# Optimization experiments

Measured on AMD Instinct MI355X. Metric: run time of the kernel, lower is better.

Reference implementation:

```python
import jax, jax.numpy as jnp
import numpy as np

B, L, D, H = 8, 1024, 768, 12
UNITS, NHEADS, HDIM = 768, 12, 64
R = 0.5  # ours_force_reduction_ratio
NEG = jnp.finfo(jnp.float32).min


def setup_inputs() -> dict:
    key = jax.random.key(0)
    ks = jax.random.split(key, 12)
    hidden_states = jax.random.normal(ks[0], (B, L, D), jnp.float32)
    # HF-style extended attention mask [B,1,1,L]: 0 for valid, big negative for padding
    lengths = jax.random.randint(ks[1], (B,), L // 2, L + 1)
    pos = jnp.arange(L)
    attention_mask = jnp.where(pos[None, :] < lengths[:, None], 0.0, -1e9).astype(jnp.float32).reshape(B, 1, 1, L)
    self_attention_scores = jax.random.uniform(ks[2], (B, H, L, L), dtype=jnp.float32)
    key_layer = jax.random.normal(ks[3], (B, H, L, HDIM), jnp.float32)  # unused by forward
    tome_size = jnp.ones((B, L, 1), jnp.float32)  # unused by forward (recomputed)
    s = 0.02
    Wq = jax.random.normal(ks[4], (D, UNITS), jnp.float32) * s
    Wk = jax.random.normal(ks[5], (D, UNITS), jnp.float32) * s
    Wv = jax.random.normal(ks[6], (D, UNITS), jnp.float32) * s
    Wo = jax.random.normal(ks[7], (UNITS, D), jnp.float32) * s
    bq = jnp.zeros((UNITS,), jnp.float32)
    bk = jnp.zeros((UNITS,), jnp.float32)
    bv = jnp.zeros((UNITS,), jnp.float32)
    bo = jnp.zeros((D,), jnp.float32)
    return dict(hidden_states=hidden_states, attention_mask=attention_mask,
                self_attention_scores=self_attention_scores, key_layer=key_layer,
                tome_size=tome_size, Wq=Wq, bq=bq, Wk=Wk, bk=bk, Wv=Wv, bv=bv, Wo=Wo, bo=bo)


def _mha(q, kv, key_padding_mask, Wq, bq, Wk, bk, Wv, bv, Wo, bo):
    # standard multi-head cross attention; q: [B,Lq,D], kv: [B,L,D]
    Bq, Lq, _ = q.shape
    Q = (q @ Wq + bq).reshape(Bq, Lq, NHEADS, HDIM)
    Kp = (kv @ Wk + bk).reshape(Bq, -1, NHEADS, HDIM)
    Vp = (kv @ Wv + bv).reshape(Bq, -1, NHEADS, HDIM)
    scores = jnp.einsum('bqhd,bkhd->bhqk', Q, Kp) / jnp.sqrt(jnp.float32(HDIM))
    if key_padding_mask is not None:
        scores = jnp.where(key_padding_mask[:, None, None, :], NEG, scores)
    att = jax.nn.softmax(scores, axis=-1)
    out = jnp.einsum('bhqk,bkhd->bqhd', att, Vp).reshape(Bq, Lq, UNITS)
    return out @ Wo + bo


def reference(hidden_states, attention_mask, self_attention_scores, key_layer, tome_size,
              Wq, bq, Wk, bk, Wv, bv, Wo, bo):
    # per-sample variable K = floor(valid_len * R) - num_new_token, clamped to >= 1
    valid = (attention_mask > -10.0).astype(hidden_states.dtype)  # [B,1,1,L]
    K_list = (valid.reshape(B, L).sum(-1) * R).astype(jnp.int32)
    K_list = jnp.maximum(K_list - 1, 1)  # num_new_token == 1
    # masked_attention_scores: outer product of the 0/1 mask applied per head
    m = valid.reshape(B, L)
    scores = self_attention_scores * (m[:, :, None] * m[:, None, :])[:, None, :, :]
    imp = scores.mean(axis=1).mean(axis=1)  # mean over heads then queries -> [B,L]
    imp = imp.at[:, 0].set(jnp.inf)  # always preserve CLS
    # rank of each token in descending importance (double argsort)
    order = jnp.argsort(-imp, axis=-1)
    rank = jnp.argsort(order, axis=-1)
    keep = rank < K_list[:, None]  # [B,L]; topk_attention_mask == ~keep
    preserved_attention_mask = jnp.where(keep[:, None, None, :], attention_mask, NEG)
    # sentence pooling via softmax over the extended mask
    att = jax.nn.softmax(attention_mask, axis=-1).reshape(B, 1, L)
    sentences = jnp.einsum('bql,bld->bqd', att, hidden_states)  # [B,1,D]
    key_padding_mask = attention_mask.reshape(B, L) < -10.0
    new_token = _mha(sentences, hidden_states, key_padding_mask, Wq, bq, Wk, bk, Wv, bv, Wo, bo)
    final_token = jnp.concatenate([hidden_states, new_token], axis=1)  # [B,L+1,D]
    new_attention_mask = jnp.zeros((B, 1, 1, 1), hidden_states.dtype)
    final_attention_mask = jnp.concatenate([preserved_attention_mask, new_attention_mask], axis=-1)
    tome = jnp.ones((B, L + 1, 1), hidden_states.dtype)
    return final_token, final_attention_mask, tome
```

## Files before the change

kernel.cpp:

```cpp
#include <hip/hip_runtime.h>
#include <math.h>

#define Bb 8
#define Ll 1024
#define Dd 768
#define Hh 12
#define ROWS7 32
#define QS 8
#define SS 8
#define WSC 16
#define DC 24

#define NIMP (Bb*Hh*QS)
#define NSENT (Bb*SS)
#define NCOPY4 (Bb*Ll*Dd/4)
#define NTOME4 (Bb*(Ll+1)/4)
#define NCPYBLK ((NCOPY4 + NTOME4 + 255)/256)
#define GRID_A (NIMP + NSENT + NCPYBLK + 1)

__device__ __constant__ float NEGF_ = -3.0e38f;

#define OFF_COUNTS   0
#define OFF_QPART    256
#define OFF_QV       (OFF_QPART + DC*Bb*Dd*4)
#define OFF_U        (OFF_QV + Bb*Dd*4)
#define OFF_SBUF     (OFF_U + Bb*Hh*Dd*4)
#define OFF_SENTP    (OFF_SBUF + (size_t)Bb*Hh*Ll*4)
#define OFF_PART     (OFF_SENTP + Bb*SS*Dd*8)
#define OFF_WPART    (OFF_PART + (size_t)Bb*Hh*QS*Ll*4)
#define OFF_OPART    (OFF_WPART + (size_t)Bb*WSC*Hh*Dd*4)
#define OFF_NPART    (OFF_OPART + DC*Bb*Dd*4)

__device__ __forceinline__ int block_count256(const float* __restrict__ amask_b, int t) {
    int c = 0;
    #pragma unroll
    for (int i = 0; i < 4; ++i)
        c += (amask_b[t + 256*i] > -10.0f) ? 1 : 0;
    #pragma unroll
    for (int off = 32; off; off >>= 1) c += __shfl_xor(c, off, 64);
    __shared__ int cred[4];
    if ((t & 63) == 0) cred[t >> 6] = c;
    __syncthreads();
    return cred[0] + cred[1] + cred[2] + cred[3];
}

__global__ void kA_mega(const float4* __restrict__ scores4, const float* __restrict__ amask,
                        const float4* __restrict__ hid4,
                        float4* __restrict__ part4, double* __restrict__ sentp,
                        int* __restrict__ counts, float4* __restrict__ out4) {
    int blk = blockIdx.x;
    int t = threadIdx.x;
    if (blk < NIMP) {
        int b = blk / (Hh*QS);
        int rem = blk % (Hh*QS);
        int h = rem / QS, c = rem % QS;
        int count = block_count256(amask + b*Ll, t);
        int rpc = (count + QS - 1) / QS;
        int q0 = c*rpc, q1 = min(q0 + rpc, count);
        if (4*t >= count) return;
        const float4* base = scores4 + ((size_t)(b*Hh + h)*Ll)*(Ll/4) + t;
        float ax=0.f, ay=0.f, az=0.f, aw=0.f;
        float bx=0.f, by=0.f, bz=0.f, bw=0.f;
        int q = q0;
        #pragma unroll 4
        for (; q + 1 < q1; q += 2) {
            float4 v0 = base[(size_t)q*(Ll/4)];
            float4 v1 = base[(size_t)(q+1)*(Ll/4)];
            ax += v0.x; ay += v0.y; az += v0.z; aw += v0.w;
            bx += v1.x; by += v1.y; bz += v1.z; bw += v1.w;
        }
        if (q < q1) {
            float4 v = base[(size_t)q*(Ll/4)];
            ax += v.x; ay += v.y; az += v.z; aw += v.w;
        }
        float4 o; o.x = ax+bx; o.y = ay+by; o.z = az+bz; o.w = aw+bw;
        part4[(size_t)(b*(Hh*QS) + rem)*(Ll/4) + t] = o;
    } else if (blk < NIMP + NSENT) {
        int blk2 = blk - NIMP;
        int b = blk2 / SS, c = blk2 % SS;
        int count = block_count256(amask + b*Ll, t);
        int rpc = (count + SS - 1) / SS;
        int l0 = c*rpc, l1 = min(l0 + rpc, count);
        if (t < 192) {
            double a0=0, a1=0, a2=0, a3=0;
            const float4* base = hid4 + (size_t)b*Ll*(Dd/4) + t;
            #pragma unroll 4
            for (int l = l0; l < l1; ++l) {
                float4 v = base[(size_t)l*(Dd/4)];
                a0 += (double)v.x; a1 += (double)v.y; a2 += (double)v.z; a3 += (double)v.w;
            }
            double* o = sentp + (size_t)(b*SS + c)*Dd + 4*t;
            o[0]=a0; o[1]=a1; o[2]=a2; o[3]=a3;
        }
    } else if (blk < NIMP + NSENT + NCPYBLK) {
        int idx = (blk - NIMP - NSENT)*256 + t;
        if (idx < NCOPY4) {
            int b = idx / (Ll*Dd/4), r = idx % (Ll*Dd/4);
            out4[(size_t)b*((Ll+1)*Dd/4) + r] = hid4[idx];
        } else if (idx < NCOPY4 + NTOME4) {
            float4 one; one.x=one.y=one.z=one.w = 1.0f;
            out4[(size_t)(Bb*(Ll+1)*Dd + Bb*(Ll+1))/4 + (idx - NCOPY4)] = one;
        }
    } else {
        int w = t >> 6, lane = t & 63;
        for (int b = w; b < Bb; b += 4) {
            int c = 0;
            #pragma unroll
            for (int i = 0; i < 16; ++i)
                c += (amask[b*Ll + lane + 64*i] > -10.0f) ? 1 : 0;
            #pragma unroll
            for (int off = 32; off; off >>= 1) c += __shfl_xor(c, off, 64);
            if (lane == 0) counts[b] = c;
        }
    }
}

__global__ void kB_rank(const float* __restrict__ part, const int* __restrict__ counts,
                        const float* __restrict__ amask, float* __restrict__ out_mask) {
    __shared__ double simp[Ll];
    int blk = blockIdx.x;
    int b = blk >> 4, seg = blk & 15;
    int t = threadIdx.x;
    int count = counts[b];
    #pragma unroll
    for (int i = 0; i < 4; ++i) {
        int k = t + 256*i;
        double v;
        if (k == 0) v = 1.0e300;
        else if (k < count) {
            double s = 0.0;
            #pragma unroll 4
            for (int j = 0; j < Hh*QS; ++j)
                s += (double)part[(size_t)(b*(Hh*QS) + j)*Ll + k];
            v = s * (1.0/12288.0);
        } else v = 0.0;
        simp[k] = v;
    }
    __syncthreads();
    int K = max((count >> 1) - 1, 1);
    int ti = seg*64 + (t >> 2);
    int prt = t & 3;
    double mv = simp[ti];
    int cnt = 0;
    int l0 = prt*256;
    #pragma unroll 4
    for (int j = 0; j < 256; ++j) {
        int l = l0 + j;
        double v = simp[l];
        cnt += (v > mv || (v == mv && l < ti)) ? 1 : 0;
    }
    cnt += __shfl_xor(cnt, 1, 64);
    cnt += __shfl_xor(cnt, 2, 64);
    if (prt == 0)
        out_mask[b*(Ll+1) + ti] = (cnt < K) ? amask[b*Ll + ti] : NEGF_;
    if (seg == 0 && t == 0) out_mask[b*(Ll+1) + Ll] = 0.0f;
}

__global__ void kC_qpart(const double* __restrict__ sentp, const int* __restrict__ counts,
                         const float* __restrict__ Wq, float* __restrict__ qpart) {
    __shared__ float s_lds[Bb][32];
    int blk = blockIdx.x, t = threadIdx.x;
    int d0 = blk*32;
    {
        int b = t >> 5, dd = t & 31;
        double s = 0.0;
        #pragma unroll
        for (int c = 0; c < SS; ++c)
            s += sentp[(size_t)(b*SS + c)*Dd + d0 + dd];
        s_lds[b][dd] = (float)(s / (double)counts[b]);
    }
    __syncthreads();
    float acc[Bb][3];
    #pragma unroll
    for (int b = 0; b < Bb; ++b) { acc[b][0]=0.f; acc[b][1]=0.f; acc[b][2]=0.f; }
    #pragma unroll 4
    for (int dd = 0; dd < 32; ++dd) {
        const float* wr = Wq + (size_t)(d0 + dd)*Dd;
        float w0 = wr[t], w1 = wr[t+256], w2 = wr[t+512];
        #pragma unroll
        for (int b = 0; b < Bb; ++b) {
            float sv = s_lds[b][dd];
            acc[b][0] += sv*w0; acc[b][1] += sv*w1; acc[b][2] += sv*w2;
        }
    }
    #pragma unroll
    for (int b = 0; b < Bb; ++b) {
        float* o = qpart + (size_t)(blk*Bb + b)*Dd;
        o[t] = acc[b][0]; o[t+256] = acc[b][1]; o[t+512] = acc[b][2];
    }
}

__global__ void kD_u(const float* __restrict__ qpart, const float* __restrict__ bq,
                     const float* __restrict__ Wk,
                     float* __restrict__ Qv, float* __restrict__ u) {
    __shared__ float q_lds[64];
    int blk = blockIdx.x; int b = blk / Hh, h = blk % Hh;
    int t = threadIdx.x;
    if (t < 64) {
        int j = h*64 + t;
        float s = 0.f;
        #pragma unroll
        for (int c = 0; c < DC; ++c) s += qpart[(size_t)(c*Bb + b)*Dd + j];
        s += bq[j];
        q_lds[t] = s;
        Qv[b*Dd + j] = s;
    }
    __syncthreads();
    #pragma unroll
    for (int i = 0; i < 3; ++i) {
        int d = t + 256*i;
        const float* wr = Wk + (size_t)d*Dd + h*64;
        float acc = 0.f;
        #pragma unroll
        for (int j = 0; j < 64; ++j) acc += wr[j]*q_lds[j];
        u[(size_t)(b*Hh + h)*Dd + d] = acc;
    }
}

__global__ void kE_scores(const float4* __restrict__ hid4, const float4* __restrict__ u4,
                          const float* __restrict__ Qv, const float* __restrict__ bk,
                          const int* __restrict__ counts, float* __restrict__ sbuf) {
    __shared__ float4 u_lds[Hh*192];
    __shared__ float qbk[Hh];
    int blk = blockIdx.x;
    int b = blk / (Ll/ROWS7);
    int kc = blk % (Ll/ROWS7);
    int t = threadIdx.x;
    for (int i = t; i < Hh*192; i += 256) u_lds[i] = u4[(size_t)b*Hh*192 + i];
    if (t < Hh) {
        float a = 0.f;
        for (int j = 0; j < 64; ++j) a += Qv[b*Dd + t*64 + j] * bk[t*64 + j];
        qbk[t] = a;
    }
    __syncthreads();
    int count = counts[b];
    int wave = t >> 6, lane = t & 63;
    #pragma unroll
    for (int r = 0; r < ROWS7/4; ++r) {
        int k = kc*ROWS7 + wave + 4*r;
        const float4* hr4 = hid4 + (size_t)(b*Ll + k)*(Dd/4) + lane;
        float a[Hh];
        #pragma unroll
        for (int h = 0; h < Hh; ++h) a[h] = 0.f;
        #pragma unroll
        for (int i = 0; i < 3; ++i) {
            float4 v = hr4[i*64];
            #pragma unroll
            for (int h = 0; h < Hh; ++h) {
                float4 uv = u_lds[h*192 + i*64 + lane];
                a[h] += v.x*uv.x + v.y*uv.y + v.z*uv.z + v.w*uv.w;
            }
        }
        #pragma unroll
        for (int h = 0; h < Hh; ++h) {
            #pragma unroll
            for (int off = 32; off; off >>= 1) a[h] += __shfl_xor(a[h], off, 64);
        }
        #pragma unroll
        for (int h = 0; h < Hh; ++h) {
            if (lane == h) {
                sbuf[(size_t)(b*Hh + h)*Ll + k] =
                    (k < count) ? (a[h] + qbk[h]) * 0.125f : -1.0e30f;
            }
        }
    }
}

__global__ void kF_softmax(float* __restrict__ sbuf) {
    __shared__ float redmax[4];
    __shared__ float redsum[4];
    int blk = blockIdx.x, t = threadIdx.x;
    float* s = sbuf + (size_t)blk * Ll;
    int wave = t >> 6, lane = t & 63;
    float v0 = s[t], v1 = s[t+256], v2 = s[t+512], v3 = s[t+768];
    float mx = fmaxf(fmaxf(v0, v1), fmaxf(v2, v3));
    #pragma unroll
    for (int off = 32; off; off >>= 1) mx = fmaxf(mx, __shfl_xor(mx, off, 64));
    if (lane == 0) redmax[wave] = mx;
    __syncthreads();
    mx = fmaxf(fmaxf(redmax[0], redmax[1]), fmaxf(redmax[2], redmax[3]));
    float e0 = expf(v0-mx), e1 = expf(v1-mx), e2 = expf(v2-mx), e3 = expf(v3-mx);
    float sum = e0+e1+e2+e3;
    #pragma unroll
    for (int off = 32; off; off >>= 1) sum += __shfl_xor(sum, off, 64);
    if (lane == 0) redsum[wave] = sum;
    __syncthreads();
    sum = redsum[0]+redsum[1]+redsum[2]+redsum[3];
    s[t]     = e0/sum;
    s[t+256] = e1/sum;
    s[t+512] = e2/sum;
    s[t+768] = e3/sum;
}

__global__ void kG_wpart(const float4* __restrict__ hid4, const float* __restrict__ att,
                         const int* __restrict__ counts, float4* __restrict__ wpart4) {
    __shared__ float att_s[Hh][64];
    int blk = blockIdx.x;
    int b = blk / WSC, c = blk % WSC;
    int count = counts[b];
    int rpc = (count + WSC - 1) / WSC;
    int l0 = c*rpc, l1 = min(l0 + rpc, count);
    int nl = l1 - l0;
    int t = threadIdx.x;
    for (int idx = t; idx < Hh*64; idx += 192) {
        int h = idx >> 6, ll = idx & 63;
        att_s[h][ll] = (ll < nl) ? att[(size_t)(b*Hh + h)*Ll + l0 + ll] : 0.f;
    }
    __syncthreads();
    float4 acc[Hh];
    #pragma unroll
    for (int h = 0; h < Hh; ++h) { acc[h].x=0.f; acc[h].y=0.f; acc[h].z=0.f; acc[h].w=0.f; }
    const float4* base = hid4 + (size_t)b*Ll*(Dd/4) + t;
    #pragma unroll 2
    for (int l = 0; l < nl; ++l) {
        float4 v = base[(size_t)(l0 + l)*(Dd/4)];
        #pragma unroll
        for (int h = 0; h < Hh; ++h) {
            float ah = att_s[h][l];
            acc[h].x += ah*v.x; acc[h].y += ah*v.y; acc[h].z += ah*v.z; acc[h].w += ah*v.w;
        }
    }
    #pragma unroll
    for (int h = 0; h < Hh; ++h)
        wpart4[((size_t)(b*WSC + c)*Hh + h)*(Dd/4) + t] = acc[h];
}

__global__ void kH_opart(const float* __restrict__ wpart, const float* __restrict__ Wv,
                         float* __restrict__ opart) {
    __shared__ float w_lds[Bb][Hh][32];
    int blk = blockIdx.x, t = threadIdx.x;
    int d0 = blk*32;
    for (int idx = t; idx < Bb*Hh*32; idx += 256) {
        int b = idx / (Hh*32);
        int rem = idx % (Hh*32);
        int h = rem >> 5, dd = rem & 31;
        float s = 0.f;
        #pragma unroll
        for (int c = 0; c < WSC; ++c)
            s += wpart[((size_t)(b*WSC + c)*Hh + h)*Dd + d0 + dd];
        w_lds[b][h][dd] = s;
    }
    __syncthreads();
    int j0 = t, j1 = t+256, j2 = t+512;
    int h0 = j0 >> 6, h1 = j1 >> 6, h2 = j2 >> 6;
    float acc[Bb][3];
    #pragma unroll
    for (int b = 0; b < Bb; ++b) { acc[b][0]=0.f; acc[b][1]=0.f; acc[b][2]=0.f; }
    #pragma unroll 4
    for (int dd = 0; dd < 32; ++dd) {
        const float* wr = Wv + (size_t)(d0 + dd)*Dd;
        float w0 = wr[j0], w1 = wr[j1], w2 = wr[j2];
        #pragma unroll
        for (int b = 0; b < Bb; ++b) {
            acc[b][0] += w_lds[b][h0][dd]*w0;
            acc[b][1] += w_lds[b][h1][dd]*w1;
            acc[b][2] += w_lds[b][h2][dd]*w2;
        }
    }
    #pragma unroll
    for (int b = 0; b < Bb; ++b) {
        float* o = opart + (size_t)(blk*Bb + b)*Dd;
        o[j0] = acc[b][0]; o[j1] = acc[b][1]; o[j2] = acc[b][2];
    }
}

__global__ void kI_npart(const float* __restrict__ opart, const float* __restrict__ bv,
                         const float* __restrict__ Wo, float* __restrict__ npart) {
    __shared__ float o_lds[Bb][32];
    int blk = blockIdx.x, t = threadIdx.x;
    int jr0 = blk*32;
    {
        int b = t >> 5, jj = t & 31;
        int j = jr0 + jj;
        float s = 0.f;
        #pragma unroll
        for (int c = 0; c < DC; ++c) s += opart[(size_t)(c*Bb + b)*Dd + j];
        o_lds[b][jj] = s + bv[j];
    }
    __syncthreads();
    float acc[Bb][3];
    #pragma unroll
    for (int b = 0; b < Bb; ++b) { acc[b][0]=0.f; acc[b][1]=0.f; acc[b][2]=0.f; }
    #pragma unroll 4
    for (int jj = 0; jj < 32; ++jj) {
        const float* wr = Wo + (size_t)(jr0 + jj)*Dd;
        float w0 = wr[t], w1 = wr[t+256], w2 = wr[t+512];
        #pragma unroll
        for (int b = 0; b < Bb; ++b) {
            float ov = o_lds[b][jj];
            acc[b][0] += ov*w0; acc[b][1] += ov*w1; acc[b][2] += ov*w2;
        }
    }
    #pragma unroll
    for (int b = 0; b < Bb; ++b) {
        float* o = npart + (size_t)(blk*Bb + b)*Dd;
        o[t] = acc[b][0]; o[t+256] = acc[b][1]; o[t+512] = acc[b][2];
    }
}

__global__ void kJ_final(const float* __restrict__ npart, const float* __restrict__ bo,
                         float* __restrict__ out) {
    int b = blockIdx.x, t = threadIdx.x;
    size_t base = ((size_t)b*(Ll+1) + Ll)*Dd;
    #pragma unroll
    for (int i = 0; i < 3; ++i) {
        int d = t + 256*i;
        float s = 0.f;
        #pragma unroll
        for (int c = 0; c < DC; ++c) s += npart[(size_t)(c*Bb + b)*Dd + d];
        out[base + d] = s + bo[d];
    }
}

extern "C" void kernel_launch(void* const* d_in, const int* in_sizes, int n_in,
                              void* d_out, int out_size, void* d_ws, size_t ws_size,
                              hipStream_t stream) {
    const float* hidden = (const float*)d_in[0];
    const float* amask  = (const float*)d_in[1];
    const float* scores = (const float*)d_in[2];
    const float* Wq = (const float*)d_in[5];
    const float* bq = (const float*)d_in[6];
    const float* Wk = (const float*)d_in[7];
    const float* bk = (const float*)d_in[8];
    const float* Wv = (const float*)d_in[9];
    const float* bv = (const float*)d_in[10];
    const float* Wo = (const float*)d_in[11];
    const float* bo = (const float*)d_in[12];
    float* out = (float*)d_out;

    char* ws = (char*)d_ws;
    int*    counts = (int*)   (ws + OFF_COUNTS);
    float*  qpart  = (float*) (ws + OFF_QPART);
    float*  Qv     = (float*) (ws + OFF_QV);
    float*  u      = (float*) (ws + OFF_U);
    float*  sbuf   = (float*) (ws + OFF_SBUF);
    double* sentp  = (double*)(ws + OFF_SENTP);
    float*  part   = (float*) (ws + OFF_PART);
    float*  wpart  = (float*) (ws + OFF_WPART);
    float*  opart  = (float*) (ws + OFF_OPART);
    float*  npart  = (float*) (ws + OFF_NPART);

    float* out_mask = out + (size_t)Bb*(Ll+1)*Dd;

    kA_mega   <<<GRID_A, 256, 0, stream>>>((const float4*)scores, amask,
                                           (const float4*)hidden,
                                           (float4*)part, sentp, counts, (float4*)out);
    kB_rank   <<<Bb*16, 256, 0, stream>>>(part, counts, amask, out_mask);
    kC_qpart  <<<DC, 256, 0, stream>>>(sentp, counts, Wq, qpart);
    kD_u      <<<Bb*Hh, 256, 0, stream>>>(qpart, bq, Wk, Qv, u);
    kE_scores <<<Bb*(Ll/ROWS7), 256, 0, stream>>>((const float4*)hidden, (const float4*)u,
                                                  Qv, bk, counts, sbuf);
    kF_softmax<<<Bb*Hh, 256, 0, stream>>>(sbuf);
    kG_wpart  <<<Bb*WSC, 192, 0, stream>>>((const float4*)hidden, sbuf, counts,
                                           (float4*)wpart);
    kH_opart  <<<DC, 256, 0, stream>>>(wpart, Wv, opart);
    kI_npart  <<<DC, 256, 0, stream>>>(opart, bv, Wo, npart);
    kJ_final  <<<Bb, 256, 0, stream>>>(npart, bo, out);
}
```

Baseline: 190.0 us.

## Fuse query projection into u kernel and softmax into weighted-sum kernel

Merges the Wq projection (kC) with the Wk fold (kD) so each (batch, head) block computes its own 64-wide query slice from the pooled sentence. This removes the qpart workspace round-trip and one launch. It also folds the softmax kernel into kG: each block recomputes the per-head max and sum over the score rows and normalizes on the fly, which removes another launch and the rewrite of sbuf. The cost is redundant softmax statistics across the 16 chunk blocks per batch, and a serial 24-step staged loop over Wq in each of 96 blocks.

After: 204.4 us. +7.5%, slower.

```diff
diff --git a/kernel.cpp b/kernel.cpp
--- a/kernel.cpp
+++ b/kernel.cpp
@@ -21,8 +21,7 @@
 __device__ __constant__ float NEGF_ = -3.0e38f;
 
 #define OFF_COUNTS   0
-#define OFF_QPART    256
-#define OFF_QV       (OFF_QPART + DC*Bb*Dd*4)
+#define OFF_QV       256
 #define OFF_U        (OFF_QV + Bb*Dd*4)
 #define OFF_SBUF     (OFF_U + Bb*Hh*Dd*4)
 #define OFF_SENTP    (OFF_SBUF + (size_t)Bb*Hh*Ll*4)
@@ -156,54 +155,48 @@
     if (seg == 0 && t == 0) out_mask[b*(Ll+1) + Ll] = 0.0f;
 }
 
-__global__ void kC_qpart(const double* __restrict__ sentp, const int* __restrict__ counts,
-                         const float* __restrict__ Wq, float* __restrict__ qpart) {
-    __shared__ float s_lds[Bb][32];
-    int blk = blockIdx.x, t = threadIdx.x;
-    int d0 = blk*32;
-    {
-        int b = t >> 5, dd = t & 31;
-        double s = 0.0;
-        #pragma unroll
-        for (int c = 0; c < SS; ++c)
-            s += sentp[(size_t)(b*SS + c)*Dd + d0 + dd];
-        s_lds[b][dd] = (float)(s / (double)counts[b]);
-    }
-    __syncthreads();
-    float acc[Bb][3];
-    #pragma unroll
-    for (int b = 0; b < Bb; ++b) { acc[b][0]=0.f; acc[b][1]=0.f; acc[b][2]=0.f; }
-    #pragma unroll 4
-    for (int dd = 0; dd < 32; ++dd) {
-        const float* wr = Wq + (size_t)(d0 + dd)*Dd;
-        float w0 = wr[t], w1 = wr[t+256], w2 = wr[t+512];
-        #pragma unroll
-        for (int b = 0; b < Bb; ++b) {
-            float sv = s_lds[b][dd];
-            acc[b][0] += sv*w0; acc[b][1] += sv*w1; acc[b][2] += sv*w2;
-        }
-    }
-    #pragma unroll
-    for (int b = 0; b < Bb; ++b) {
-        float* o = qpart + (size_t)(blk*Bb + b)*Dd;
-        o[t] = acc[b][0]; o[t+256] = acc[b][1]; o[t+512] = acc[b][2];
-    }
-}
-
-__global__ void kD_u(const float* __restrict__ qpart, const float* __restrict__ bq,
-                     const float* __restrict__ Wk,
-                     float* __restrict__ Qv, float* __restrict__ u) {
+__global__ void kCD_qu(const double* __restrict__ sentp, const int* __restrict__ counts,
+                       const float* __restrict__ Wq, const float* __restrict__ bq,
+                       const float* __restrict__ Wk,
+                       float* __restrict__ Qv, float* __restrict__ u) {
+    __shared__ float s_lds[Dd];
+    __shared__ float4 wstage[512];
+    __shared__ float qpart_lds[4][64];
     __shared__ float q_lds[64];
     int blk = blockIdx.x; int b = blk / Hh, h = blk % Hh;
     int t = threadIdx.x;
+    double cntd = (double)counts[b];
+    for (int i = t; i < Dd; i += 256) {
+        double s = 0.0;
+        #pragma unroll
+        for (int c = 0; c < SS; ++c) s += sentp[(size_t)(b*SS + c)*Dd + i];
+        s_lds[i] = (float)(s / cntd);
+    }
+    __syncthreads();
+    int lane = t & 63, w = t >> 6;
+    const float4* wq4 = (const float4*)Wq;
+    float qacc = 0.f;
+    for (int it = 0; it < 24; ++it) {
+        int d0 = it*32;
+        #pragma unroll
+        for (int f = t; f < 512; f += 256) {
+            int r = f >> 4, c4 = f & 15;
+            wstage[f] = wq4[(size_t)(d0 + r)*192 + h*16 + c4];
+        }
+        __syncthreads();
+        const float* wsf = (const float*)wstage;
+        #pragma unroll
+        for (int r = w*8; r < w*8 + 8; ++r)
+            qacc += s_lds[d0 + r] * wsf[r*64 + lane];
+        __syncthreads();
+    }
+    qpart_lds[w][lane] = qacc;
+    __syncthreads();
     if (t < 64) {
-        int j = h*64 + t;
-        float s = 0.f;
-        #pragma unroll
-        for (int c = 0; c < DC; ++c) s += qpart[(size_t)(c*Bb + b)*Dd + j];
-        s += bq[j];
-        q_lds[t] = s;
-        Qv[b*Dd + j] = s;
+        float q = qpart_lds[0][t] + qpart_lds[1][t] + qpart_lds[2][t]
+                + qpart_lds[3][t] + bq[h*64 + t];
+        q_lds[t] = q;
+        Qv[b*Dd + h*64 + t] = q;
     }
     __syncthreads();
     #pragma unroll
@@ -266,45 +259,40 @@
     }
 }
 
-__global__ void kF_softmax(float* __restrict__ sbuf) {
-    __shared__ float redmax[4];
-    __shared__ float redsum[4];
-    int blk = blockIdx.x, t = threadIdx.x;
-    float* s = sbuf + (size_t)blk * Ll;
-    int wave = t >> 6, lane = t & 63;
-    float v0 = s[t], v1 = s[t+256], v2 = s[t+512], v3 = s[t+768];
-    float mx = fmaxf(fmaxf(v0, v1), fmaxf(v2, v3));
-    #pragma unroll
-    for (int off = 32; off; off >>= 1) mx = fmaxf(mx, __shfl_xor(mx, off, 64));
-    if (lane == 0) redmax[wave] = mx;
-    __syncthreads();
-    mx = fmaxf(fmaxf(redmax[0], redmax[1]), fmaxf(redmax[2], redmax[3]));
-    float e0 = expf(v0-mx), e1 = expf(v1-mx), e2 = expf(v2-mx), e3 = expf(v3-mx);
-    float sum = e0+e1+e2+e3;
-    #pragma unroll
-    for (int off = 32; off; off >>= 1) sum += __shfl_xor(sum, off, 64);
-    if (lane == 0) redsum[wave] = sum;
-    __syncthreads();
-    sum = redsum[0]+redsum[1]+redsum[2]+redsum[3];
-    s[t]     = e0/sum;
-    s[t+256] = e1/sum;
-    s[t+512] = e2/sum;
-    s[t+768] = e3/sum;
-}
-
-__global__ void kG_wpart(const float4* __restrict__ hid4, const float* __restrict__ att,
-                         const int* __restrict__ counts, float4* __restrict__ wpart4) {
+__global__ void kFG_wpart(const float4* __restrict__ hid4, const float* __restrict__ sbuf,
+                          const int* __restrict__ counts, float4* __restrict__ wpart4) {
+    __shared__ float m_s[Hh], is_s[Hh];
     __shared__ float att_s[Hh][64];
     int blk = blockIdx.x;
     int b = blk / WSC, c = blk % WSC;
+    int t = threadIdx.x;
+    int wave = t >> 6, lane = t & 63;
+    #pragma unroll
+    for (int i = 0; i < 4; ++i) {
+        int h = wave*4 + i;
+        const float* s = sbuf + (size_t)(b*Hh + h)*Ll;
+        float vals[16];
+        float mx = -INFINITY;
+        #pragma unroll
+        for (int q = 0; q < 16; ++q) { vals[q] = s[lane + 64*q]; mx = fmaxf(mx, vals[q]); }
+        #pragma unroll
+        for (int off = 32; off; off >>= 1) mx = fmaxf(mx, __shfl_xor(mx, off, 64));
+        float sum = 0.f;
+        #pragma unroll
+        for (int q = 0; q < 16; ++q) sum += expf(vals[q] - mx);
+        #pragma unroll
+        for (int off = 32; off; off >>= 1) sum += __shfl_xor(sum, off, 64);
+        if (lane == 0) { m_s[h] = mx; is_s[h] = 1.f/sum; }
+    }
+    __syncthreads();
     int count = counts[b];
     int rpc = (count + WSC - 1) / WSC;
     int l0 = c*rpc, l1 = min(l0 + rpc, count);
     int nl = l1 - l0;
-    int t = threadIdx.x;
     for (int idx = t; idx < Hh*64; idx += 192) {
         int h = idx >> 6, ll = idx & 63;
-        att_s[h][ll] = (ll < nl) ? att[(size_t)(b*Hh + h)*Ll + l0 + ll] : 0.f;
+        att_s[h][ll] = (ll < nl)
+            ? expf(sbuf[(size_t)(b*Hh + h)*Ll + l0 + ll] - m_s[h]) * is_s[h] : 0.f;
     }
     __syncthreads();
     float4 acc[Hh];
@@ -430,7 +418,6 @@
 
     char* ws = (char*)d_ws;
     int*    counts = (int*)   (ws + OFF_COUNTS);
-    float*  qpart  = (float*) (ws + OFF_QPART);
     float*  Qv     = (float*) (ws + OFF_QV);
     float*  u      = (float*) (ws + OFF_U);
     float*  sbuf   = (float*) (ws + OFF_SBUF);
@@ -446,12 +433,10 @@
                                            (const float4*)hidden,
                                            (float4*)part, sentp, counts, (float4*)out);
     kB_rank   <<<Bb*16, 256, 0, stream>>>(part, counts, amask, out_mask);
-    kC_qpart  <<<DC, 256, 0, stream>>>(sentp, counts, Wq, qpart);
-    kD_u      <<<Bb*Hh, 256, 0, stream>>>(qpart, bq, Wk, Qv, u);
+    kCD_qu    <<<Bb*Hh, 256, 0, stream>>>(sentp, counts, Wq, bq, Wk, Qv, u);
     kE_scores <<<Bb*(Ll/ROWS7), 256, 0, stream>>>((const float4*)hidden, (const float4*)u,
                                                   Qv, bk, counts, sbuf);
-    kF_softmax<<<Bb*Hh, 256, 0, stream>>>(sbuf);
-    kG_wpart  <<<Bb*WSC, 192, 0, stream>>>((const float4*)hidden, sbuf, counts,
+    kFG_wpart <<<Bb*WSC, 192, 0, stream>>>((const float4*)hidden, sbuf, counts,
                                            (float4*)wpart);
     kH_opart  <<<DC, 256, 0, stream>>>(wpart, Wv, opart);
     kI_npart  <<<DC, 256, 0, stream>>>(opart, bv, Wo, npart);
```
